# Kernel tuning notes

Measured on AMD Instinct MI355X. Metric: run time of the kernel, lower is better.

Reference implementation:

```python
import jax, jax.numpy as jnp
import numpy as np

B, T, H = 262144, 15, 64


def setup_inputs() -> dict:
    key = jax.random.key(0)
    ks = jax.random.split(key, 8)
    s_ih = 1.0 / np.sqrt(H)
    return {
        "x": jax.random.normal(ks[0], (B, T), dtype=jnp.float32),
        # PyTorch GRU params: W_ih [3H, input_size=1], W_hh [3H, H], biases [3H]
        "W_ih": jax.random.uniform(ks[1], (3 * H, 1), jnp.float32, -s_ih, s_ih),
        "W_hh": jax.random.uniform(ks[2], (3 * H, H), jnp.float32, -s_ih, s_ih),
        "b_ih": jax.random.uniform(ks[3], (3 * H,), jnp.float32, -s_ih, s_ih),
        "b_hh": jax.random.uniform(ks[4], (3 * H,), jnp.float32, -s_ih, s_ih),
        "W_fc": jax.random.uniform(ks[5], (2, H), jnp.float32, -s_ih, s_ih),
        "b_fc": jax.random.uniform(ks[6], (2,), jnp.float32, -s_ih, s_ih),
    }


def reference(x, W_ih, W_hh, b_ih, b_hh, W_fc, b_fc):
    # x: [B, T]; each scalar feature is one timestep of a 1-dim GRU input.
    w_in = W_ih[:, 0]  # [3H] since input_size == 1

    def step(h, x_t):
        # x_t: [B]; input gates are just outer product with w_in (input_size=1)
        xg = x_t[:, None] * w_in[None, :] + b_ih          # [B, 3H]
        hg = h @ W_hh.T + b_hh                            # [B, 3H]
        r = jax.nn.sigmoid(xg[:, :H] + hg[:, :H])
        z = jax.nn.sigmoid(xg[:, H:2 * H] + hg[:, H:2 * H])
        n = jnp.tanh(xg[:, 2 * H:] + r * hg[:, 2 * H:])
        h_new = (1.0 - z) * n + z * h
        return h_new, None

    h0 = jnp.zeros((x.shape[0], H), dtype=x.dtype)
    h_last, _ = jax.lax.scan(step, h0, x.T)  # scan over time dim
    logits = h_last @ W_fc.T + b_fc          # [B, 2]
    return logits
```

## Files before the change

kernel.cpp:

```cpp
#include <hip/hip_runtime.h>

#define T_STEPS 15
#define ROWS_PER_BLOCK 128
#define B_TOTAL 262144
#define LOG2E 1.4426950408889634f

typedef _Float16 half8 __attribute__((ext_vector_type(8)));
typedef _Float16 half4 __attribute__((ext_vector_type(4)));
typedef __fp16   fp16x2 __attribute__((ext_vector_type(2)));
typedef float f32x4 __attribute__((ext_vector_type(4)));

#define MFMA_INIT(acc, a, b, cz) \
    asm("v_mfma_f32_16x16x32_f16 %0, %1, %2, %3" : "=&v"(acc) : "v"(a), "v"(b), "v"(cz))
#define MFMA_ACC(acc, a, b) \
    asm("v_mfma_f32_16x16x32_f16 %0, %1, %2, %0" : "+v"(acc) : "v"(a), "v"(b))

__device__ __forceinline__ int swz(int row, int e) {
    return (row * 64 + e) ^ ((row & 7) << 3);
}

#define MFMA_BLOCK(S, AP0, AP1)  do { \
    int ofA = bytesS0, ofB = bytesS1; \
    asm volatile("" : "+v"(ofA), "+v"(ofB)); \
    const char* bp0 = wbase + ofA; \
    const char* bp1 = wbase + ofB; \
    half8 A0 = *(const half8*)(AP0); \
    half8 A1 = *(const half8*)(AP1); \
    _Pragma("unroll") \
    for (int tq = 0; tq < 4; ++tq) { \
        half8 Br0 = *(const half8*)(bp0 + tq * 2048); \
        half8 Br1 = *(const half8*)(bp1 + tq * 2048); \
        half8 Bz0 = *(const half8*)(bp0 + (4 + tq) * 2048); \
        half8 Bz1 = *(const half8*)(bp1 + (4 + tq) * 2048); \
        half8 Bn0 = *(const half8*)(bp0 + (8 + tq) * 2048); \
        half8 Bn1 = *(const half8*)(bp1 + (8 + tq) * 2048); \
        MFMA_INIT(accr[S][tq], A0, Br0, zero4); \
        MFMA_ACC (accr[S][tq], A1, Br1); \
        MFMA_INIT(accz[S][tq], A0, Bz0, zero4); \
        MFMA_ACC (accz[S][tq], A1, Bz1); \
        MFMA_INIT(accn[S][tq], A0, Bn0, zero4); \
        MFMA_ACC (accn[S][tq], A1, Bn1); \
        if (tq < 3) __builtin_amdgcn_sched_barrier(0); \
    } \
} while (0)

#define HAZPAD() do { \
    __builtin_amdgcn_sched_barrier(0); \
    asm volatile("s_nop 7"); \
    __builtin_amdgcn_sched_barrier(0); \
} while (0)

#define GATES(S, TT) do { \
    f32x4 xt4 = *(const f32x4*)&xlds[(TT) * ROWS_PER_BLOCK + wave * 32 + (S) * 16 + g4 * 4]; \
    _Pragma("unroll") \
    for (int reg = 0; reg < 4; ++reg) { \
        float xt = xt4[reg]; \
        float hnv[4]; \
        _Pragma("unroll") \
        for (int tq = 0; tq < 4; ++tq) { \
            float pr = accr[S][tq][reg] + __builtin_fmaf(xt, wihr[tq], sr[tq]); \
            float er = __builtin_amdgcn_exp2f(-pr); \
            float rg = __builtin_amdgcn_rcpf(1.0f + er); \
            float pz = accz[S][tq][reg] + __builtin_fmaf(xt, wihz[tq], sz[tq]); \
            float ez = __builtin_amdgcn_exp2f(-pz); \
            float na = __builtin_fmaf(rg, accn[S][tq][reg], \
                        __builtin_fmaf(rg, seedn[tq], \
                         __builtin_fmaf(xt, wihn[tq], bihn[tq]))); \
            float en = __builtin_amdgcn_exp2f(-na); \
            float A_ = 1.0f + en; \
            float C_ = 1.0f + ez; \
            float R_ = __builtin_amdgcn_rcpf(A_ * C_); \
            float P_ = __builtin_fmaf(-en, ez, ez); \
            float hn = __builtin_fmaf(h[S][tq][reg], A_, P_) * R_; \
            h[S][tq][reg] = hn; \
            hnv[tq] = hn; \
        } \
        fp16x2 h01 = __builtin_amdgcn_cvt_pkrtz(hnv[0], hnv[1]); \
        fp16x2 h23 = __builtin_amdgcn_cvt_pkrtz(hnv[2], hnv[3]); \
        half4 vh; \
        vh[0] = (_Float16)h01[0]; vh[1] = (_Float16)h01[1]; \
        vh[2] = (_Float16)h23[0]; vh[3] = (_Float16)h23[1]; \
        *(half4*)wr[S][reg] = vh; \
    } \
} while (0)

__global__ __launch_bounds__(256, 2) void gru_mfma_kernel(
    const float* __restrict__ x,
    const float* __restrict__ W_ih,
    const float* __restrict__ W_hh,
    const float* __restrict__ b_ih,
    const float* __restrict__ b_hh,
    const float* __restrict__ W_fc,
    const float* __restrict__ b_fc,
    float* __restrict__ out)
{
    __shared__ _Float16 wlds[192 * 64];
    __shared__ float    xlds[T_STEPS * ROWS_PER_BLOCK];
    __shared__ _Float16 hst[8][16 * 64];

    const int tid  = threadIdx.x;
    const int wave = tid >> 6;
    const int lane = tid & 63;
    const int c    = lane & 15;
    const int g4   = lane >> 4;
    const int r0   = blockIdx.x * ROWS_PER_BLOCK;

    for (int idx = tid; idx < 192 * 64; idx += 256) {
        int n = idx >> 6, s = idx & 63;
        int korig = (s & 3) * 16 + (s >> 2);
        float scale = (n < 128) ? LOG2E : (2.0f * LOG2E);
        wlds[swz(n, s)] = (_Float16)(W_hh[n * 64 + korig] * scale);
    }
    for (int idx = tid; idx < ROWS_PER_BLOCK * T_STEPS; idx += 256) {
        int row = idx / T_STEPS, t = idx - row * T_STEPS;
        xlds[t * ROWS_PER_BLOCK + row] = x[r0 * T_STEPS + idx];
    }
    __syncthreads();

    float wihr[4], wihz[4], wihn[4], sr[4], sz[4], seedn[4], bihn[4];
#pragma unroll
    for (int tq = 0; tq < 4; ++tq) {
        int jn = tq * 16 + c;
        wihr[tq]  = W_ih[jn] * LOG2E;
        wihz[tq]  = W_ih[64 + jn] * LOG2E;
        wihn[tq]  = W_ih[128 + jn] * (2.0f * LOG2E);
        sr[tq]    = (b_ih[jn] + b_hh[jn]) * LOG2E;
        sz[tq]    = (b_ih[64 + jn] + b_hh[64 + jn]) * LOG2E;
        seedn[tq] = b_hh[128 + jn] * (2.0f * LOG2E);
        bihn[tq]  = b_ih[128 + jn] * (2.0f * LOG2E);
    }

    const int eS0 = c * 64 + (((g4 * 8) + 0)  ^ ((c & 7) << 3));
    const int eS1 = c * 64 + (((g4 * 8) + 32) ^ ((c & 7) << 3));
    const int bytesS0 = eS0 * 2;
    const int bytesS1 = eS1 * 2;
    const _Float16* aA0 = &hst[wave * 2 + 0][eS0];
    const _Float16* aA1 = &hst[wave * 2 + 0][eS1];
    const _Float16* aB0 = &hst[wave * 2 + 1][eS0];
    const _Float16* aB1 = &hst[wave * 2 + 1][eS1];
    _Float16* wr[2][4];
#pragma unroll
    for (int s = 0; s < 2; ++s)
#pragma unroll
        for (int reg = 0; reg < 4; ++reg) {
            int row = g4 * 4 + reg;
            wr[s][reg] = &hst[wave * 2 + s][row * 64 + ((c * 4) ^ ((row & 7) << 3))];
        }

    const f32x4 zero4 = (f32x4){0.0f, 0.0f, 0.0f, 0.0f};

    f32x4 accr[2][4], accz[2][4], accn[2][4];
#pragma unroll
    for (int s = 0; s < 2; ++s)
#pragma unroll
        for (int tq = 0; tq < 4; ++tq) {
            accr[s][tq] = zero4;
            accz[s][tq] = zero4;
            accn[s][tq] = zero4;
        }

    float h[2][4][4];
#pragma unroll
    for (int s = 0; s < 2; ++s)
#pragma unroll
        for (int tq = 0; tq < 4; ++tq)
#pragma unroll
            for (int reg = 0; reg < 4; ++reg) h[s][tq][reg] = 0.0f;

    const char* wbase = (const char*)&wlds[0];

    GATES(0, 0);
    MFMA_BLOCK(0, aA0, aA1);
    GATES(1, 0);

#pragma unroll 1
    for (int t = 1; t < T_STEPS - 1; ++t) {
        MFMA_BLOCK(1, aB0, aB1);
        HAZPAD();
        GATES(0, t);
        MFMA_BLOCK(0, aA0, aA1);
        HAZPAD();
        GATES(1, t);
    }
    MFMA_BLOCK(1, aB0, aB1);
    HAZPAD();
    GATES(0, T_STEPS - 1);
    GATES(1, T_STEPS - 1);

    const float* wfc = W_fc;
    const float* bfc = b_fc;
    asm volatile("" : "+v"(wfc), "+v"(bfc));
    float wfc0[4], wfc1[4];
#pragma unroll
    for (int tq = 0; tq < 4; ++tq) {
        wfc0[tq] = wfc[tq * 16 + c];
        wfc1[tq] = wfc[64 + tq * 16 + c];
    }
#pragma unroll
    for (int s = 0; s < 2; ++s)
#pragma unroll
    for (int reg = 0; reg < 4; ++reg) {
        float s0 = 0.0f, s1 = 0.0f;
#pragma unroll
        for (int tq = 0; tq < 4; ++tq) {
            s0 = __builtin_fmaf(h[s][tq][reg], wfc0[tq], s0);
            s1 = __builtin_fmaf(h[s][tq][reg], wfc1[tq], s1);
        }
#pragma unroll
        for (int m = 1; m < 16; m <<= 1) {
            s0 += __shfl_xor(s0, m, 64);
            s1 += __shfl_xor(s1, m, 64);
        }
        if (c == 0) {
            int gr = r0 + wave * 32 + s * 16 + g4 * 4 + reg;
            out[gr * 2 + 0] = s0 + bfc[0];
            out[gr * 2 + 1] = s1 + bfc[1];
        }
    }
}

extern "C" void kernel_launch(void* const* d_in, const int* in_sizes, int n_in,
                              void* d_out, int out_size, void* d_ws, size_t ws_size,
                              hipStream_t stream) {
    const float* x    = (const float*)d_in[0];
    const float* W_ih = (const float*)d_in[1];
    const float* W_hh = (const float*)d_in[2];
    const float* b_ih = (const float*)d_in[3];
    const float* b_hh = (const float*)d_in[4];
    const float* W_fc = (const float*)d_in[5];
    const float* b_fc = (const float*)d_in[6];
    float* out = (float*)d_out;

    dim3 grid(B_TOTAL / ROWS_PER_BLOCK);
    dim3 block(256);
    gru_mfma_kernel<<<grid, block, 0, stream>>>(x, W_ih, W_hh, b_ih, b_hh, W_fc, b_fc, out);
}
```

Baseline: 208.5 us.

## Interleave MFMA of one sub-tile with gate math of the other

Replaces the separate MFMA-block and gate-evaluation phases with a fused schedule. Each chunk issues the MFMAs for one 16-row sub-tile between slices of sigmoid/tanh gate evaluation for the other sub-tile. W_hh fragment loads from LDS are double-buffered one chunk ahead, and most explicit s_nop hazard padding is dropped. The aim is to hide MFMA latency and LDS load latency behind the transcendental VALU work inside a single wave. The cost is higher register pressure from the double buffers, and the code now relies on enough independent instructions between dependent MFMA results and VALU reads to avoid hazards.

Result: faster. 200.6 us (-3.8%).

```diff
diff --git a/kernel.cpp b/kernel.cpp
--- a/kernel.cpp
+++ b/kernel.cpp
@@ -15,72 +15,94 @@
 #define MFMA_ACC(acc, a, b) \
     asm("v_mfma_f32_16x16x32_f16 %0, %1, %2, %0" : "+v"(acc) : "v"(a), "v"(b))
 
+#define SB() __builtin_amdgcn_sched_barrier(0)
+
 __device__ __forceinline__ int swz(int row, int e) {
     return (row * 64 + e) ^ ((row & 7) << 3);
 }
 
-#define MFMA_BLOCK(S, AP0, AP1)  do { \
+#define GEVAL(SG, RG, TQ, XT) do { \
+    float pr = accr[SG][TQ][RG] + __builtin_fmaf(XT, wihr[TQ], sr[TQ]); \
+    float er = __builtin_amdgcn_exp2f(-pr); \
+    float rg_ = __builtin_amdgcn_rcpf(1.0f + er); \
+    float pz = accz[SG][TQ][RG] + __builtin_fmaf(XT, wihz[TQ], sz[TQ]); \
+    float ez = __builtin_amdgcn_exp2f(-pz); \
+    float na = __builtin_fmaf(rg_, accn[SG][TQ][RG], \
+                __builtin_fmaf(rg_, seedn[TQ], \
+                 __builtin_fmaf(XT, wihn[TQ], bihn[TQ]))); \
+    float en = __builtin_amdgcn_exp2f(-na); \
+    float A_ = 1.0f + en; \
+    float C_ = 1.0f + ez; \
+    float R_ = __builtin_amdgcn_rcpf(A_ * C_); \
+    float P_ = __builtin_fmaf(-en, ez, ez); \
+    float hn = __builtin_fmaf(h[SG][TQ][RG], A_, P_) * R_; \
+    h[SG][TQ][RG] = hn; \
+    hnv[TQ] = hn; \
+} while (0)
+
+#define PACKWRITE(SG, RG) do { \
+    fp16x2 h01 = __builtin_amdgcn_cvt_pkrtz(hnv[0], hnv[1]); \
+    fp16x2 h23 = __builtin_amdgcn_cvt_pkrtz(hnv[2], hnv[3]); \
+    half4 vh; \
+    vh[0] = (_Float16)h01[0]; vh[1] = (_Float16)h01[1]; \
+    vh[2] = (_Float16)h23[0]; vh[3] = (_Float16)h23[1]; \
+    *(half4*)wr[SG][RG] = vh; \
+} while (0)
+
+#define LD6(buf, KK) do { \
+    buf[0] = *(const half8*)(bp0 + (KK) * 2048); \
+    buf[1] = *(const half8*)(bp1 + (KK) * 2048); \
+    buf[2] = *(const half8*)(bp0 + (4 + (KK)) * 2048); \
+    buf[3] = *(const half8*)(bp1 + (4 + (KK)) * 2048); \
+    buf[4] = *(const half8*)(bp0 + (8 + (KK)) * 2048); \
+    buf[5] = *(const half8*)(bp1 + (8 + (KK)) * 2048); \
+} while (0)
+
+#define CHUNK(SM, SG, K, BCUR, PREF) do { \
+    float hnv[4]; \
+    float XT = xt4[K]; \
+    PREF; \
+    SB(); \
+    MFMA_INIT(accr[SM][K], A0, BCUR[0], zero4); \
+    MFMA_INIT(accz[SM][K], A0, BCUR[2], zero4); \
+    MFMA_INIT(accn[SM][K], A0, BCUR[4], zero4); \
+    SB(); \
+    GEVAL(SG, K, 0, XT); GEVAL(SG, K, 1, XT); \
+    SB(); \
+    MFMA_ACC(accr[SM][K], A1, BCUR[1]); \
+    MFMA_ACC(accz[SM][K], A1, BCUR[3]); \
+    MFMA_ACC(accn[SM][K], A1, BCUR[5]); \
+    SB(); \
+    GEVAL(SG, K, 2, XT); GEVAL(SG, K, 3, XT); \
+    PACKWRITE(SG, K); \
+    SB(); \
+} while (0)
+
+#define FUSED(SM, SG, TT) do { \
     int ofA = bytesS0, ofB = bytesS1; \
     asm volatile("" : "+v"(ofA), "+v"(ofB)); \
     const char* bp0 = wbase + ofA; \
     const char* bp1 = wbase + ofB; \
-    half8 A0 = *(const half8*)(AP0); \
-    half8 A1 = *(const half8*)(AP1); \
+    half8 A0 = *(const half8*)((SM) ? aB0 : aA0); \
+    half8 A1 = *(const half8*)((SM) ? aB1 : aA1); \
+    f32x4 xt4 = *(const f32x4*)&xlds[(TT) * ROWS_PER_BLOCK + wave * 32 + (SG) * 16 + g4 * 4]; \
+    half8 Bf0[6], Bf1[6]; \
+    LD6(Bf0, 0); \
+    CHUNK(SM, SG, 0, Bf0, LD6(Bf1, 1)); \
+    CHUNK(SM, SG, 1, Bf1, LD6(Bf0, 2)); \
+    CHUNK(SM, SG, 2, Bf0, LD6(Bf1, 3)); \
+    CHUNK(SM, SG, 3, Bf1, (void)0); \
+} while (0)
+
+#define GATES_PLAIN(SG, TT) do { \
+    f32x4 xt4 = *(const f32x4*)&xlds[(TT) * ROWS_PER_BLOCK + wave * 32 + (SG) * 16 + g4 * 4]; \
     _Pragma("unroll") \
-    for (int tq = 0; tq < 4; ++tq) { \
-        half8 Br0 = *(const half8*)(bp0 + tq * 2048); \
-        half8 Br1 = *(const half8*)(bp1 + tq * 2048); \
-        half8 Bz0 = *(const half8*)(bp0 + (4 + tq) * 2048); \
-        half8 Bz1 = *(const half8*)(bp1 + (4 + tq) * 2048); \
-        half8 Bn0 = *(const half8*)(bp0 + (8 + tq) * 2048); \
-        half8 Bn1 = *(const half8*)(bp1 + (8 + tq) * 2048); \
-        MFMA_INIT(accr[S][tq], A0, Br0, zero4); \
-        MFMA_ACC (accr[S][tq], A1, Br1); \
-        MFMA_INIT(accz[S][tq], A0, Bz0, zero4); \
-        MFMA_ACC (accz[S][tq], A1, Bz1); \
-        MFMA_INIT(accn[S][tq], A0, Bn0, zero4); \
-        MFMA_ACC (accn[S][tq], A1, Bn1); \
-        if (tq < 3) __builtin_amdgcn_sched_barrier(0); \
-    } \
-} while (0)
-
-#define HAZPAD() do { \
-    __builtin_amdgcn_sched_barrier(0); \
-    asm volatile("s_nop 7"); \
-    __builtin_amdgcn_sched_barrier(0); \
-} while (0)
-
-#define GATES(S, TT) do { \
-    f32x4 xt4 = *(const f32x4*)&xlds[(TT) * ROWS_PER_BLOCK + wave * 32 + (S) * 16 + g4 * 4]; \
-    _Pragma("unroll") \
-    for (int reg = 0; reg < 4; ++reg) { \
-        float xt = xt4[reg]; \
+    for (int rg2 = 0; rg2 < 4; ++rg2) { \
         float hnv[4]; \
-        _Pragma("unroll") \
-        for (int tq = 0; tq < 4; ++tq) { \
-            float pr = accr[S][tq][reg] + __builtin_fmaf(xt, wihr[tq], sr[tq]); \
-            float er = __builtin_amdgcn_exp2f(-pr); \
-            float rg = __builtin_amdgcn_rcpf(1.0f + er); \
-            float pz = accz[S][tq][reg] + __builtin_fmaf(xt, wihz[tq], sz[tq]); \
-            float ez = __builtin_amdgcn_exp2f(-pz); \
-            float na = __builtin_fmaf(rg, accn[S][tq][reg], \
-                        __builtin_fmaf(rg, seedn[tq], \
-                         __builtin_fmaf(xt, wihn[tq], bihn[tq]))); \
-            float en = __builtin_amdgcn_exp2f(-na); \
-            float A_ = 1.0f + en; \
-            float C_ = 1.0f + ez; \
-            float R_ = __builtin_amdgcn_rcpf(A_ * C_); \
-            float P_ = __builtin_fmaf(-en, ez, ez); \
-            float hn = __builtin_fmaf(h[S][tq][reg], A_, P_) * R_; \
-            h[S][tq][reg] = hn; \
-            hnv[tq] = hn; \
-        } \
-        fp16x2 h01 = __builtin_amdgcn_cvt_pkrtz(hnv[0], hnv[1]); \
-        fp16x2 h23 = __builtin_amdgcn_cvt_pkrtz(hnv[2], hnv[3]); \
-        half4 vh; \
-        vh[0] = (_Float16)h01[0]; vh[1] = (_Float16)h01[1]; \
-        vh[2] = (_Float16)h23[0]; vh[3] = (_Float16)h23[1]; \
-        *(half4*)wr[S][reg] = vh; \
+        float XT = xt4[rg2]; \
+        GEVAL(SG, rg2, 0, XT); GEVAL(SG, rg2, 1, XT); \
+        GEVAL(SG, rg2, 2, XT); GEVAL(SG, rg2, 3, XT); \
+        PACKWRITE(SG, rg2); \
     } \
 } while (0)
 
@@ -169,23 +191,18 @@
 
     const char* wbase = (const char*)&wlds[0];
 
-    GATES(0, 0);
-    MFMA_BLOCK(0, aA0, aA1);
-    GATES(1, 0);
+    GATES_PLAIN(0, 0);
+    FUSED(0, 1, 0);
 
 #pragma unroll 1
     for (int t = 1; t < T_STEPS - 1; ++t) {
-        MFMA_BLOCK(1, aB0, aB1);
-        HAZPAD();
-        GATES(0, t);
-        MFMA_BLOCK(0, aA0, aA1);
-        HAZPAD();
-        GATES(1, t);
-    }
-    MFMA_BLOCK(1, aB0, aB1);
-    HAZPAD();
-    GATES(0, T_STEPS - 1);
-    GATES(1, T_STEPS - 1);
+        FUSED(1, 0, t);
+        FUSED(0, 1, t);
+    }
+
+    FUSED(1, 0, T_STEPS - 1);
+    SB(); asm volatile("s_nop 7"); SB();
+    GATES_PLAIN(1, T_STEPS - 1);
 
     const float* wfc = W_fc;
     const float* bfc = b_fc;
```
